# Kernel optimization log

Hardware: AMD Instinct MI355X
Metric: run time of the kernel (lower is better)

The kernel has to match this reference:

```python
import jax, jax.numpy as jnp
import numpy as np

C = 192; WS = 8; SHIFT = 4; NH = 6; HD = 32; N = WS * WS; EPS = 1e-5


def _cpb_table(ws):
    r = np.arange(-(ws - 1), ws, dtype=np.float32)
    t = np.stack(np.meshgrid(r, r, indexing='ij'), axis=-1) / (ws - 1) * 8.0
    t = np.sign(t) * np.log2(np.abs(t) + 1.0) / np.log2(8.0)
    return t.reshape(-1, 2)  # ((2ws-1)^2, 2)


def _rel_index(ws):
    c = np.stack(np.meshgrid(np.arange(ws), np.arange(ws), indexing='ij')).reshape(2, -1)
    rel = (c[:, :, None] - c[:, None, :]).transpose(1, 2, 0).astype(np.int64)
    rel[..., 0] += ws - 1; rel[..., 1] += ws - 1; rel[..., 0] *= 2 * ws - 1
    return rel.sum(-1)  # (N, N)


def _attn_mask(H, W, ws, shift):
    img = np.zeros((H, W), np.float32); cnt = 0.0
    sl = (slice(0, -ws), slice(-ws, -shift), slice(-shift, None))
    for hs in sl:
        for wsl in sl:
            img[hs, wsl] = cnt; cnt += 1.0
    m = img.reshape(H // ws, ws, W // ws, ws).transpose(0, 2, 1, 3).reshape(-1, ws * ws)
    d = m[:, None, :] - m[:, :, None]
    return np.where(d != 0, -100.0, 0.0).astype(np.float32)  # (nW, N, N)


def _ln(x, g, b):
    mu = jnp.mean(x, -1, keepdims=True)
    var = jnp.mean((x - mu) ** 2, -1, keepdims=True)
    return (x - mu) / jnp.sqrt(var + EPS) * g + b


def setup_inputs() -> dict:
    key = jax.random.key(0)
    ks = jax.random.split(key, 8)
    H = W = 384
    w = lambda k, s: jax.random.normal(k, s, jnp.float32) * 0.05
    return {
        'hidden_states': jax.random.normal(ks[0], (1, H * W, C), jnp.float32),
        'q_w': w(ks[1], (C, C)), 'q_b': jnp.zeros((C,), jnp.float32),
        'k_w': w(ks[2], (C, C)),
        'v_w': w(ks[3], (C, C)), 'v_b': jnp.zeros((C,), jnp.float32),
        'logit_scale': jnp.full((NH, 1, 1), np.log(10.0), jnp.float32),
        'cpb_w1': w(ks[4], (2, 512)), 'cpb_b1': jnp.zeros((512,), jnp.float32),
        'cpb_w2': w(ks[5], (512, NH)),
        'proj_w': w(ks[6], (C, C)), 'proj_b': jnp.zeros((C,), jnp.float32),
        'ln1_g': jnp.ones((C,), jnp.float32), 'ln1_b': jnp.zeros((C,), jnp.float32),
        'fc1_w': w(ks[7], (C, 2 * C)), 'fc1_b': jnp.zeros((2 * C,), jnp.float32),
        'fc2_w': w(jax.random.fold_in(key, 9), (2 * C, C)), 'fc2_b': jnp.zeros((C,), jnp.float32),
        'ln2_g': jnp.ones((C,), jnp.float32), 'ln2_b': jnp.zeros((C,), jnp.float32),
        'height': 384, 'width': 384,
    }


def reference(hidden_states, q_w, q_b, k_w, v_w, v_b, logit_scale, cpb_w1, cpb_b1,
              cpb_w2, proj_w, proj_b, ln1_g, ln1_b, fc1_w, fc1_b, fc2_w, fc2_b,
              ln2_g, ln2_b, height, width):
    B = hidden_states.shape[0]
    shortcut = hidden_states
    x = hidden_states.reshape(B, height, width, C)
    # shift
    x = jnp.roll(x, (-SHIFT, -SHIFT), (1, 2))
    # window partition -> (B*nW, N, C)
    win = x.reshape(B, height // WS, WS, width // WS, WS, C).transpose(0, 1, 3, 2, 4, 5).reshape(-1, N, C)
    q = (win @ q_w + q_b).reshape(-1, N, NH, HD).transpose(0, 2, 1, 3)
    k = (win @ k_w).reshape(-1, N, NH, HD).transpose(0, 2, 1, 3)
    v = (win @ v_w + v_b).reshape(-1, N, NH, HD).transpose(0, 2, 1, 3)
    # cosine attention
    qn = q / jnp.maximum(jnp.linalg.norm(q, axis=-1, keepdims=True), 1e-12)
    kn = k / jnp.maximum(jnp.linalg.norm(k, axis=-1, keepdims=True), 1e-12)
    scale = jnp.exp(jnp.minimum(logit_scale, jnp.log(100.0))).reshape(1, NH, 1, 1)
    scores = jnp.einsum('whnd,whmd->whnm', qn, kn) * scale
    # continuous relative position bias via MLP
    table = jnp.asarray(_cpb_table(WS))
    bias_tab = jax.nn.relu(table @ cpb_w1 + cpb_b1) @ cpb_w2  # (169, NH)
    idx = jnp.asarray(_rel_index(WS)).reshape(-1)
    rpb = bias_tab[idx].reshape(N, N, NH).transpose(2, 0, 1)
    rpb = 16.0 * jax.nn.sigmoid(rpb)
    mask = jnp.asarray(_attn_mask(height, width, WS, SHIFT))  # (nW, N, N)
    # NOTE: source adds the mask twice (faithful reproduction)
    scores = scores + rpb[None] + 2.0 * mask[:, None]
    probs = jax.nn.softmax(scores, -1)
    ctx = jnp.einsum('whnm,whmd->whnd', probs, v).transpose(0, 2, 1, 3).reshape(-1, N, C)
    attn = ctx @ proj_w + proj_b
    # window reverse + unshift
    x = attn.reshape(B, height // WS, width // WS, WS, WS, C).transpose(0, 1, 3, 2, 4, 5).reshape(B, height, width, C)
    x = jnp.roll(x, (SHIFT, SHIFT), (1, 2)).reshape(B, height * width, C)
    # post-norm residual (Swin v2 style)
    h = shortcut + _ln(x, ln1_g, ln1_b)
    mlp = jax.nn.gelu(h @ fc1_w + fc1_b, approximate=False) @ fc2_w + fc2_b
    return h + _ln(mlp, ln2_g, ln2_b)
```

## Files before the change

kernel.cpp:

```cpp
#include <hip/hip_runtime.h>
#include <hip/hip_bf16.h>
#include <math.h>

typedef __hip_bfloat16 bf16;
typedef __attribute__((ext_vector_type(8))) short short8;
typedef __attribute__((ext_vector_type(4))) float floatx4;
typedef unsigned int u32;

#define NTOK 147456
#define IMG 384

__device__ __forceinline__ int gather_row(int m) {
    int gw = m >> 6, t = m & 63;
    int wr = gw / 48, wc = gw - wr * 48;
    int hh = wr * 8 + (t >> 3);
    int ww = wc * 8 + (t & 7);
    int oh = hh + 4; if (oh >= IMG) oh -= IMG;
    int ow = ww + 4; if (ow >= IMG) ow -= IMG;
    return oh * IMG + ow;
}

__device__ __forceinline__ unsigned short f2bu(float f) {
    unsigned u = __float_as_uint(f);
    unsigned r = (u + 0x7fffu + ((u >> 16) & 1u)) >> 16;
    return (unsigned short)r;
}
__device__ __forceinline__ float bu2f(unsigned short u) {
    return __uint_as_float(((unsigned)u) << 16);
}

__device__ __forceinline__ float gelu_fast(float x) {
    const float z = fabsf(x) * 0.70710678118654752f;
    const float t = __builtin_amdgcn_rcpf(fmaf(0.3275911f, z, 1.0f));
    float p = fmaf(1.061405429f, t, -1.453152027f);
    p = fmaf(p, t, 1.421413741f);
    p = fmaf(p, t, -0.284496736f);
    p = fmaf(p, t, 0.254829592f);
    p *= t;
    const float e = __expf(-z * z);
    float erfv = fmaf(-p, e, 1.0f);
    erfv = (x < 0.0f) ? -erfv : erfv;
    return 0.5f * x * (1.0f + erfv);
}

__device__ __forceinline__ void async_copy16(void* lds, const void* g) {
    __builtin_amdgcn_global_load_lds(
        (const __attribute__((address_space(1))) u32*)g,
        (__attribute__((address_space(3))) u32*)lds,
        16, 0, 0);
}


__global__ __launch_bounds__(256)
void conv_pack(const float* __restrict__ hidden, bf16* __restrict__ Apk)
{
    const int cid = blockIdx.x * 256 + threadIdx.x;
    const int mtG = cid / 384;
    const int rest = cid - mtG * 384;
    const int kg = rest >> 4, mm = rest & 15;
    const int tok = mtG * 16 + mm;
    const float* p = hidden + (size_t)gather_row(tok) * 192 + kg * 8;
    const float4 a = *(const float4*)p;
    const float4 b = *(const float4*)(p + 4);
    short8 o;
    o[0] = (short)f2bu(a.x); o[1] = (short)f2bu(a.y);
    o[2] = (short)f2bu(a.z); o[3] = (short)f2bu(a.w);
    o[4] = (short)f2bu(b.x); o[5] = (short)f2bu(b.y);
    o[6] = (short)f2bu(b.z); o[7] = (short)f2bu(b.w);
    *(short8*)(Apk + (size_t)cid * 8) = o;
}

__global__ __launch_bounds__(256)
void pack_w(const float* __restrict__ W, bf16* __restrict__ out, int K, int N)
{
    const int cid = blockIdx.x * 256 + threadIdx.x;
    const int KG = K >> 3;
    const int total = (N >> 4) * KG * 16;
    if (cid >= total) return;
    const int n = cid & 15;
    const int kg = (cid >> 4) % KG;
    const int ntG = (cid >> 4) / KG;
    short8 o;
#pragma unroll
    for (int j = 0; j < 8; ++j)
        o[j] = (short)f2bu(W[(size_t)(kg * 8 + j) * N + ntG * 16 + n]);
    *(short8*)(out + (size_t)cid * 8) = o;
}

__global__ __launch_bounds__(256)
void fuse_bias(const float* __restrict__ qb, const float* __restrict__ vb,
               float* __restrict__ out)
{
    const int t = blockIdx.x * 256 + threadIdx.x;
    if (t >= 576) return;
    out[t] = (t < 192) ? qb[t] : ((t < 384) ? 0.0f : vb[t - 384]);
}

#define EPI_NONE 0
#define EPI_GELU 1

template<int KDIM, bool PACK_OUT, int EPI, int KGOUT, int MW>
__global__ __launch_bounds__(256, MW)
void gemm_mfma(const bf16* __restrict__ Apk, const bf16* __restrict__ Bpk,
               const float* __restrict__ bias, bf16* __restrict__ C, int N)
{
    constexpr int KG = KDIM / 8;
    constexpr int KT = KDIM / 32;
    constexpr int KC = KDIM / 192;
    __shared__ __align__(16) char sB[2][24576];
    const int tid = threadIdx.x;
    const int wave = tid >> 6, lane = tid & 63;
    const int bm = blockIdx.x * 128;
    const int NPo = N / 64;
    const char* Bsrc = (const char*)Bpk;

    short8 areg[2][KT];
    {
        const char* Asrc = (const char*)Apk;
#pragma unroll
        for (int x = 0; x < 2; ++x) {
            const size_t rowb = (size_t)((bm >> 4) + wave * 2 + x) * KG * 256;
#pragma unroll
            for (int kt = 0; kt < KT; ++kt)
                areg[x][kt] = *(const short8*)(Asrc + rowb + (size_t)kt * 1024 + lane * 16);
        }
    }

    auto stage = [&](int npo_, int kc_, int bufp) {
#pragma unroll
        for (int i = 0; i < 6; ++i) {
            const int cid = i * 256 + wave * 64 + lane;
            const int nt = cid / 384, off = cid - nt * 384;
            const char* g = Bsrc + ((size_t)((npo_ * 4 + nt) * KG + kc_ * 24) * 256 + (size_t)off * 16);
            async_copy16(sB[bufp] + (i * 256 + wave * 64) * 16, g);
        }
    };

    stage(0, 0, 0);

    for (int npo = 0; npo < NPo; ++npo) {
        floatx4 acc[8];
#pragma unroll
        for (int f = 0; f < 8; ++f)
            acc[f] = (floatx4){0.f, 0.f, 0.f, 0.f};

#pragma unroll
        for (int kc = 0; kc < KC; ++kc) {
            const int p = npo * KC + kc;
            const int buf = p & 1;
            const bool last = (npo == NPo - 1) && (kc == KC - 1);
            if (!last) {
                if (kc < KC - 1) stage(npo, kc + 1, buf ^ 1);
                else             stage(npo + 1, 0, buf ^ 1);
                asm volatile("s_waitcnt vmcnt(6)" ::: "memory");
            } else {
                asm volatile("s_waitcnt vmcnt(0)" ::: "memory");
            }
            __builtin_amdgcn_sched_barrier(0);
            asm volatile("s_barrier" ::: "memory");

            char* sb = sB[buf];
#pragma unroll
            for (int kt6 = 0; kt6 < 6; ++kt6) {
                const short8 a0 = areg[0][kc * 6 + kt6];
                const short8 a1 = areg[1][kc * 6 + kt6];
#pragma unroll
                for (int nt = 0; nt < 4; ++nt) {
                    const short8 b = *(const short8*)(sb + nt * 6144 + kt6 * 1024 + lane * 16);
                    acc[nt]     = __builtin_amdgcn_mfma_f32_16x16x32_bf16(a0, b, acc[nt],     0, 0, 0);
                    acc[4 + nt] = __builtin_amdgcn_mfma_f32_16x16x32_bf16(a1, b, acc[4 + nt], 0, 0, 0);
                }
            }
            if (kc < KC - 1)
                asm volatile("s_barrier" ::: "memory");
        }

        {
            const int ebuf = (npo * KC + KC - 1) & 1;
            asm volatile("s_barrier" ::: "memory");
            char* wb = sB[ebuf] + wave * 4608;
#pragma unroll
            for (int m2 = 0; m2 < 2; ++m2) {
#pragma unroll
                for (int nt = 0; nt < 4; ++nt) {
                    const floatx4 v = acc[m2 * 4 + nt];
                    const int c = nt * 16 + (lane & 15);
                    const float bval = bias ? bias[npo * 64 + c] : 0.0f;
#pragma unroll
                    for (int i = 0; i < 4; ++i) {
                        float f = v[i] + bval;
                        if (EPI == EPI_GELU)
                            f = gelu_fast(f);
                        const int r = m2 * 16 + (lane >> 4) * 4 + i;
                        *(unsigned short*)(wb + (r * 72 + c) * 2) = f2bu(f);
                    }
                }
            }
            asm volatile("s_waitcnt lgkmcnt(0)" ::: "memory");
            asm volatile("s_barrier" ::: "memory");
            if (PACK_OUT) {
                const int m = lane >> 1, c2 = (lane & 1) * 32;
                const int grow = bm + wave * 32 + m;
#pragma unroll
                for (int i = 0; i < 4; ++i) {
                    const short8 row = *(const short8*)(wb + (m * 72 + c2 + i * 8) * 2);
                    const int gcol = npo * 64 + c2 + i * 8;
                    bf16* dst = C + ((size_t)((grow >> 4) * KGOUT + (gcol >> 3)) * 16 + (grow & 15)) * 8;
                    *(short8*)dst = row;
                }
            } else {
                const int mr = lane >> 3, c2 = (lane & 7) * 8;
#pragma unroll
                for (int i = 0; i < 4; ++i) {
                    const int rr = i * 8 + mr;
                    const short8 row = *(const short8*)(wb + (rr * 72 + c2) * 2);
                    bf16* dst = C + (size_t)(bm + wave * 32 + rr) * N + npo * 64 + c2;
                    *(short8*)dst = row;
                }
            }
            asm volatile("s_barrier" ::: "memory");
        }
    }
}


__device__ __forceinline__ float cpb_coord(int i) {
    float a = (float)(i - 7) * (8.0f / 7.0f);
    float s = (a > 0.f) ? 1.f : ((a < 0.f) ? -1.f : 0.f);
    return s * log2f(fabsf(a) + 1.0f) * (1.0f / 3.0f);
}

__global__ __launch_bounds__(512)
void cpb_mlp(const float* __restrict__ w1, const float* __restrict__ b1,
             const float* __restrict__ w2, float* __restrict__ tab)
{
    const int r = blockIdx.x;
    const int t = threadIdx.x;
    const float x0 = cpb_coord(r / 15);
    const float x1 = cpb_coord(r % 15);
    const float hgt = fmaxf(x0 * w1[t] + x1 * w1[512 + t] + b1[t], 0.0f);
    __shared__ float red[512];
    for (int n = 0; n < 6; ++n) {
        red[t] = hgt * w2[t * 6 + n];
        __syncthreads();
        for (int s = 256; s > 0; s >>= 1) {
            if (t < s) red[t] += red[t + s];
            __syncthreads();
        }
        if (t == 0) tab[r * 6 + n] = red[0];
        __syncthreads();
    }
}

__global__ __launch_bounds__(256)
void rpb_expand(const float* __restrict__ tab, float* __restrict__ rpb)
{
    const int idx = blockIdx.x * 256 + threadIdx.x;
    if (idx >= 6 * 4096) return;
    const int h = idx >> 12;
    const int t = (idx >> 6) & 63;
    const int j = idx & 63;
    const int pr = t >> 3, pc = t & 7, qr = j >> 3, qc = j & 7;
    const int ridx = (pr - qr + 7) * 15 + (pc - qc + 7);
    const float v = tab[ridx * 6 + h];
    rpb[idx] = 16.0f / (1.0f + expf(-v));
}

__global__ __launch_bounds__(256, 2)
void attn_mfma(const bf16* __restrict__ QKV, const float* __restrict__ rpb,
               const float* __restrict__ logit_scale, bf16* __restrict__ Ctx)
{
    __shared__ __align__(16) char lds[4][9216];
    const int wave = threadIdx.x >> 6, lane = threadIdx.x & 63;
    const int l15 = lane & 15, quad = lane >> 4;
    const int wh = blockIdx.x * 4 + wave;
    const int w = wh / 6, h = wh - w * 6;
    char* Pb = lds[wave];
    char* Vt = lds[wave] + 4608;

    const bf16* wbase = QKV + (size_t)w * 64 * 576;

    {
        const bf16* vp = wbase + (size_t)lane * 576 + 384 + h * 32;
        const short8 v0 = *(const short8*)(vp);
        const short8 v1 = *(const short8*)(vp + 8);
        const short8 v2 = *(const short8*)(vp + 16);
        const short8 v3 = *(const short8*)(vp + 24);
#pragma unroll
        for (int j = 0; j < 8; ++j) {
            *(short*)(Vt + ((j     ) * 72 + lane) * 2) = v0[j];
            *(short*)(Vt + ((j +  8) * 72 + lane) * 2) = v1[j];
            *(short*)(Vt + ((j + 16) * 72 + lane) * 2) = v2[j];
            *(short*)(Vt + ((j + 24) * 72 + lane) * 2) = v3[j];
        }
    }

    const int wr = w / 48, wc = w - wr * 48;
    const bool edge = (wr == 47) || (wc == 47);
    int rid_j[4];
    if (edge) {
#pragma unroll
        for (int jt = 0; jt < 4; ++jt) {
            const int t = jt * 16 + l15;
            const int rr = (wr == 47) ? (((t >> 3) < 4) ? 1 : 2) : 0;
            const int rc = (wc == 47) ? (((t & 7) < 4) ? 1 : 2) : 0;
            rid_j[jt] = rr * 3 + rc;
        }
    }

    short8 bfrag[4];
#pragma unroll
    for (int jt = 0; jt < 4; ++jt) {
        const short8 raw = *(const short8*)(wbase + (size_t)(jt * 16 + l15) * 576 + 192 + h * 32 + quad * 8);
        float f[8]; float ss = 0.f;
#pragma unroll
        for (int j = 0; j < 8; ++j) { f[j] = bu2f((unsigned short)raw[j]); ss += f[j] * f[j]; }
        ss += __shfl_xor(ss, 16); ss += __shfl_xor(ss, 32);
        const float rn = 1.0f / fmaxf(sqrtf(ss), 1e-12f);
        short8 o;
#pragma unroll
        for (int j = 0; j < 8; ++j) o[j] = (short)f2bu(f[j] * rn);
        bfrag[jt] = o;
    }

    floatx4 acc[4][4];
#pragma unroll
    for (int it = 0; it < 4; ++it)
#pragma unroll
        for (int jt = 0; jt < 4; ++jt)
            acc[it][jt] = (floatx4){0.f, 0.f, 0.f, 0.f};
#pragma unroll
    for (int it = 0; it < 4; ++it) {
        const short8 raw = *(const short8*)(wbase + (size_t)(it * 16 + l15) * 576 + h * 32 + quad * 8);
        float f[8]; float ss = 0.f;
#pragma unroll
        for (int j = 0; j < 8; ++j) { f[j] = bu2f((unsigned short)raw[j]); ss += f[j] * f[j]; }
        ss += __shfl_xor(ss, 16); ss += __shfl_xor(ss, 32);
        const float rn = 1.0f / fmaxf(sqrtf(ss), 1e-12f);
        short8 afr;
#pragma unroll
        for (int j = 0; j < 8; ++j) afr[j] = (short)f2bu(f[j] * rn);
#pragma unroll
        for (int jt = 0; jt < 4; ++jt)
            acc[it][jt] = __builtin_amdgcn_mfma_f32_16x16x32_bf16(afr, bfrag[jt], acc[it][jt], 0, 0, 0);
    }

    const float scale = __expf(fminf(logit_scale[h], 4.6051701859880914f));
    const float* rpbh = rpb + h * 4096;

#pragma unroll
    for (int it = 0; it < 4; ++it) {
#pragma unroll
        for (int r = 0; r < 4; ++r) {
            const int i = it * 16 + quad * 4 + r;
            int rid_i = 0;
            if (edge) {
                const int rr = (wr == 47) ? (((i >> 3) < 4) ? 1 : 2) : 0;
                const int rc = (wc == 47) ? (((i & 7) < 4) ? 1 : 2) : 0;
                rid_i = rr * 3 + rc;
            }
#pragma unroll
            for (int jt = 0; jt < 4; ++jt) {
                float v = acc[it][jt][r] * scale + rpbh[i * 64 + jt * 16 + l15];
                if (edge && rid_i != rid_j[jt]) v -= 200.0f;
                acc[it][jt][r] = v;
            }
        }
    }

    float inv[4][4];
#pragma unroll
    for (int it = 0; it < 4; ++it) {
#pragma unroll
        for (int r = 0; r < 4; ++r) {
            float m = fmaxf(fmaxf(acc[it][0][r], acc[it][1][r]),
                            fmaxf(acc[it][2][r], acc[it][3][r]));
            m = fmaxf(m, __shfl_xor(m, 1)); m = fmaxf(m, __shfl_xor(m, 2));
            m = fmaxf(m, __shfl_xor(m, 4)); m = fmaxf(m, __shfl_xor(m, 8));
            float s = 0.f;
#pragma unroll
            for (int jt = 0; jt < 4; ++jt) {
                const float e = __expf(acc[it][jt][r] - m);
                acc[it][jt][r] = e; s += e;
            }
            s += __shfl_xor(s, 1); s += __shfl_xor(s, 2);
            s += __shfl_xor(s, 4); s += __shfl_xor(s, 8);
            inv[it][r] = 1.0f / s;
        }
    }

    floatx4 ctx[4][2];
#pragma unroll
    for (int it = 0; it < 4; ++it)
#pragma unroll
        for (int dt = 0; dt < 2; ++dt)
            ctx[it][dt] = (floatx4){0.f, 0.f, 0.f, 0.f};

#pragma unroll
    for (int ks = 0; ks < 2; ++ks) {
#pragma unroll
        for (int it = 0; it < 4; ++it)
#pragma unroll
            for (int jl = 0; jl < 2; ++jl)
#pragma unroll
                for (int r = 0; r < 4; ++r) {
                    const int i = it * 16 + quad * 4 + r;
                    *(short*)(Pb + (i * 36 + jl * 16 + l15) * 2) =
                        (short)f2bu(acc[it][ks * 2 + jl][r]);
                }
#pragma unroll
        for (int it = 0; it < 4; ++it) {
            const short8 pf = *(const short8*)(Pb + ((it * 16 + l15) * 36 + quad * 8) * 2);
#pragma unroll
            for (int dt = 0; dt < 2; ++dt) {
                const short8 vf = *(const short8*)(Vt + ((dt * 16 + l15) * 72 + ks * 32 + quad * 8) * 2);
                ctx[it][dt] = __builtin_amdgcn_mfma_f32_16x16x32_bf16(pf, vf, ctx[it][dt], 0, 0, 0);
            }
        }
    }

#pragma unroll
    for (int it = 0; it < 4; ++it)
#pragma unroll
        for (int dt = 0; dt < 2; ++dt)
#pragma unroll
            for (int r = 0; r < 4; ++r) {
                const int i = it * 16 + quad * 4 + r;
                *(short*)(Pb + (i * 36 + dt * 16 + l15) * 2) =
                    (short)f2bu(ctx[it][dt][r] * inv[it][r]);
            }

    const int tok = w * 64 + lane;
    const size_t obase = ((size_t)(tok >> 4) * 24 + h * 4) * 128 + (size_t)(tok & 15) * 8;
#pragma unroll
    for (int c = 0; c < 4; ++c) {
        const short8 row = *(const short8*)(Pb + (lane * 36 + c * 8) * 2);
        *(short8*)(Ctx + obase + (size_t)c * 128) = row;
    }
}


__global__ __launch_bounds__(256)
void ln_h(const bf16* __restrict__ X, const float* __restrict__ hidden,
          const float* __restrict__ g, const float* __restrict__ b,
          bf16* __restrict__ Hres, bf16* __restrict__ Hpk)
{
    const int lane = threadIdx.x & 63;
    const int wv = threadIdx.x >> 6;
    const int tok = blockIdx.x * 4 + wv;
    const int grow = gather_row(tok);
    __shared__ float rows[4][192];
    const bf16* xr = X + (size_t)tok * 192;
    const float x0 = bu2f(*(const unsigned short*)(xr + lane));
    const float x1 = bu2f(*(const unsigned short*)(xr + lane + 64));
    const float x2 = bu2f(*(const unsigned short*)(xr + lane + 128));
    float s = x0 + x1 + x2;
#pragma unroll
    for (int o = 32; o > 0; o >>= 1) s += __shfl_xor(s, o);
    const float mean = s * (1.0f / 192.0f);
    const float d0 = x0 - mean, d1 = x1 - mean, d2 = x2 - mean;
    float vsum = d0 * d0 + d1 * d1 + d2 * d2;
#pragma unroll
    for (int o = 32; o > 0; o >>= 1) vsum += __shfl_xor(vsum, o);
    const float rstd = rsqrtf(vsum * (1.0f / 192.0f) + 1e-5f);
    const float* hr = hidden + (size_t)grow * 192;
    const float h0 = hr[lane]       + d0 * rstd * g[lane]       + b[lane];
    const float h1 = hr[lane + 64]  + d1 * rstd * g[lane + 64]  + b[lane + 64];
    const float h2 = hr[lane + 128] + d2 * rstd * g[lane + 128] + b[lane + 128];
    bf16* hres = Hres + (size_t)tok * 192;
    *(unsigned short*)(hres + lane)       = f2bu(h0);
    *(unsigned short*)(hres + lane + 64)  = f2bu(h1);
    *(unsigned short*)(hres + lane + 128) = f2bu(h2);
    rows[wv][lane] = h0; rows[wv][lane + 64] = h1; rows[wv][lane + 128] = h2;
    __syncthreads();
    if (lane < 24) {
        short8 o;
#pragma unroll
        for (int j = 0; j < 8; ++j) o[j] = (short)f2bu(rows[wv][lane * 8 + j]);
        const int mtG = tok >> 4, mm = tok & 15;
        *(short8*)(Hpk + ((size_t)(mtG * 24 + lane) * 16 + mm) * 8) = o;
    }
}

__global__ __launch_bounds__(256)
void ln_out(const bf16* __restrict__ Y, const bf16* __restrict__ Hres,
            const float* __restrict__ g, const float* __restrict__ b,
            float* __restrict__ Out)
{
    const int lane = threadIdx.x & 63;
    const int tok = blockIdx.x * 4 + (threadIdx.x >> 6);
    const int grow = gather_row(tok);
    const bf16* yr = Y + (size_t)tok * 192;
    const float x0 = bu2f(*(const unsigned short*)(yr + lane));
    const float x1 = bu2f(*(const unsigned short*)(yr + lane + 64));
    const float x2 = bu2f(*(const unsigned short*)(yr + lane + 128));
    float s = x0 + x1 + x2;
#pragma unroll
    for (int o = 32; o > 0; o >>= 1) s += __shfl_xor(s, o);
    const float mean = s * (1.0f / 192.0f);
    const float d0 = x0 - mean, d1 = x1 - mean, d2 = x2 - mean;
    float vsum = d0 * d0 + d1 * d1 + d2 * d2;
#pragma unroll
    for (int o = 32; o > 0; o >>= 1) vsum += __shfl_xor(vsum, o);
    const float rstd = rsqrtf(vsum * (1.0f / 192.0f) + 1e-5f);
    const bf16* hr = Hres + (size_t)tok * 192;
    float* op = Out + (size_t)grow * 192;
    op[lane]       = bu2f(*(const unsigned short*)(hr + lane))       + d0 * rstd * g[lane]       + b[lane];
    op[lane + 64]  = bu2f(*(const unsigned short*)(hr + lane + 64))  + d1 * rstd * g[lane + 64]  + b[lane + 64];
    op[lane + 128] = bu2f(*(const unsigned short*)(hr + lane + 128)) + d2 * rstd * g[lane + 128] + b[lane + 128];
}


extern "C" void kernel_launch(void* const* d_in, const int* in_sizes, int n_in,
                              void* d_out, int out_size, void* d_ws, size_t ws_size,
                              hipStream_t stream)
{
    const float* hidden = (const float*)d_in[0];
    const float* q_w = (const float*)d_in[1];
    const float* q_b = (const float*)d_in[2];
    const float* k_w = (const float*)d_in[3];
    const float* v_w = (const float*)d_in[4];
    const float* v_b = (const float*)d_in[5];
    const float* logit_scale = (const float*)d_in[6];
    const float* cpb_w1 = (const float*)d_in[7];
    const float* cpb_b1 = (const float*)d_in[8];
    const float* cpb_w2 = (const float*)d_in[9];
    const float* proj_w = (const float*)d_in[10];
    const float* proj_b = (const float*)d_in[11];
    const float* ln1_g = (const float*)d_in[12];
    const float* ln1_b = (const float*)d_in[13];
    const float* fc1_w = (const float*)d_in[14];
    const float* fc1_b = (const float*)d_in[15];
    const float* fc2_w = (const float*)d_in[16];
    const float* fc2_b = (const float*)d_in[17];
    const float* ln2_g = (const float*)d_in[18];
    const float* ln2_b = (const float*)d_in[19];

    char* ws = (char*)d_ws;
    bf16*  APK   = (bf16*)(ws + 0);
    float* RPB   = (float*)(ws + 0);
    bf16*  PROJW = (bf16*)(ws + (1 << 20));
    bf16*  MID   = (bf16*)(ws + 0);
    bf16*  CTX   = (bf16*)(ws + 56623104);
    bf16*  QKVW  = (bf16*)(ws + 56623104);
    float* QKVB  = (float*)(ws + 56844288);
    float* TAB   = (float*)(ws + 56846592);
    bf16*  QKV   = (bf16*)(ws + 113246208);
    bf16*  HRES  = (bf16*)(ws + 113246208);
    bf16*  HPK   = (bf16*)(ws + 169869312);
    bf16*  Y     = (bf16*)(ws + 226492416);
    bf16*  X     = (bf16*)(ws + 283115520);
    bf16*  FC1W  = (bf16*)(ws + 283115520);
    bf16*  FC2W  = (bf16*)(ws + 283262976);
    float* OUT   = (float*)d_out;

    cpb_mlp<<<225, 512, 0, stream>>>(cpb_w1, cpb_b1, cpb_w2, TAB);
    fuse_bias<<<3, 256, 0, stream>>>(q_b, v_b, QKVB);
    pack_w<<<18, 256, 0, stream>>>(q_w, QKVW,                 192, 192);
    pack_w<<<18, 256, 0, stream>>>(k_w, QKVW + 12 * 24 * 128, 192, 192);
    pack_w<<<18, 256, 0, stream>>>(v_w, QKVW + 24 * 24 * 128, 192, 192);
    conv_pack<<<13824, 256, 0, stream>>>(hidden, APK);

    gemm_mfma<192, false, EPI_NONE, 1, 3><<<1152, 256, 0, stream>>>(APK, QKVW, QKVB, QKV, 576);

    rpb_expand<<<96, 256, 0, stream>>>(TAB, RPB);
    pack_w<<<18, 256, 0, stream>>>(proj_w, PROJW, 192, 192);

    attn_mfma<<<3456, 256, 0, stream>>>(QKV, RPB, logit_scale, CTX);

    gemm_mfma<192, false, EPI_NONE, 1, 3><<<1152, 256, 0, stream>>>(CTX, PROJW, proj_b, X, 192);

    ln_h<<<NTOK / 4, 256, 0, stream>>>(X, hidden, ln1_g, ln1_b, HRES, HPK);

    pack_w<<<36, 256, 0, stream>>>(fc1_w, FC1W, 192, 384);
    pack_w<<<36, 256, 0, stream>>>(fc2_w, FC2W, 384, 192);

    gemm_mfma<192, true, EPI_GELU, 48, 3><<<1152, 256, 0, stream>>>(HPK, FC1W, fc1_b, MID, 384);
    gemm_mfma<384, false, EPI_NONE, 1, 2><<<1152, 256, 0, stream>>>(MID, FC2W, fc2_b, Y, 192);

    ln_out<<<NTOK / 4, 256, 0, stream>>>(Y, HRES, ln2_g, ln2_b, OUT);
}
```

Before: 652.7 us.

## Fold q/k normalization into scores and drop softmax max pass

The attention kernel no longer normalizes Q and K in registers before the MFMA. It feeds raw bf16 Q/K and applies the row and column inverse norms and the logit scale to the score afterwards. The softmax max-reduction is replaced by a constant shift (scale+16) precomputed into the rpb table, which is valid because cosine scores are bounded. Packed bf16 conversions replace scalar rounding, and the GEMM waitcnt thresholds are relaxed to overlap more loads. This trades some accuracy (unnormalized bf16 inputs, fixed softmax offset) for fewer ALU ops and shuffles.

```diff
diff --git a/kernel.cpp b/kernel.cpp
--- a/kernel.cpp
+++ b/kernel.cpp
@@ -27,6 +27,12 @@
 }
 __device__ __forceinline__ float bu2f(unsigned short u) {
     return __uint_as_float(((unsigned)u) << 16);
+}
+
+__device__ __forceinline__ u32 cvt_pk_bf16(float lo, float hi) {
+    u32 r;
+    asm("v_cvt_pk_bf16_f32 %0, %1, %2" : "=v"(r) : "v"(lo), "v"(hi));
+    return r;
 }
 
 __device__ __forceinline__ float gelu_fast(float x) {
@@ -152,9 +158,13 @@
             if (!last) {
                 if (kc < KC - 1) stage(npo, kc + 1, buf ^ 1);
                 else             stage(npo + 1, 0, buf ^ 1);
-                asm volatile("s_waitcnt vmcnt(6)" ::: "memory");
+                if (kc == 0 && npo > 0)
+                    asm volatile("s_waitcnt vmcnt(10)" ::: "memory");
+                else
+                    asm volatile("s_waitcnt vmcnt(6)" ::: "memory");
             } else {
-                asm volatile("s_waitcnt vmcnt(0)" ::: "memory");
+                if (KC == 1) asm volatile("s_waitcnt vmcnt(4)" ::: "memory");
+                else         asm volatile("s_waitcnt vmcnt(0)" ::: "memory");
             }
             __builtin_amdgcn_sched_barrier(0);
             asm volatile("s_barrier" ::: "memory");
@@ -253,7 +263,8 @@
 }
 
 __global__ __launch_bounds__(256)
-void rpb_expand(const float* __restrict__ tab, float* __restrict__ rpb)
+void rpb_expand(const float* __restrict__ tab, const float* __restrict__ logit_scale,
+                float* __restrict__ rpb)
 {
     const int idx = blockIdx.x * 256 + threadIdx.x;
     if (idx >= 6 * 4096) return;
@@ -263,7 +274,8 @@
     const int pr = t >> 3, pc = t & 7, qr = j >> 3, qc = j & 7;
     const int ridx = (pr - qr + 7) * 15 + (pc - qc + 7);
     const float v = tab[ridx * 6 + h];
-    rpb[idx] = 16.0f / (1.0f + expf(-v));
+    const float scale = __expf(fminf(logit_scale[h], 4.6051701859880914f));
+    rpb[idx] = 16.0f / (1.0f + expf(-v)) - scale - 16.0f;
 }
 
 __global__ __launch_bounds__(256, 2)
@@ -308,22 +320,25 @@
         }
     }
 
-    short8 bfrag[4];
+    const float scale = __expf(fminf(logit_scale[h], 4.6051701859880914f));
+
+    short8 kfr[4];
+    float rnk[4];
 #pragma unroll
     for (int jt = 0; jt < 4; ++jt) {
-        const short8 raw = *(const short8*)(wbase + (size_t)(jt * 16 + l15) * 576 + 192 + h * 32 + quad * 8);
-        float f[8]; float ss = 0.f;
-#pragma unroll
-        for (int j = 0; j < 8; ++j) { f[j] = bu2f((unsigned short)raw[j]); ss += f[j] * f[j]; }
+        kfr[jt] = *(const short8*)(wbase + (size_t)(jt * 16 + l15) * 576 + 192 + h * 32 + quad * 8);
+        float ss = 0.f;
+#pragma unroll
+        for (int j = 0; j < 8; ++j) {
+            const float f = bu2f((unsigned short)kfr[jt][j]);
+            ss = fmaf(f, f, ss);
+        }
         ss += __shfl_xor(ss, 16); ss += __shfl_xor(ss, 32);
-        const float rn = 1.0f / fmaxf(sqrtf(ss), 1e-12f);
-        short8 o;
-#pragma unroll
-        for (int j = 0; j < 8; ++j) o[j] = (short)f2bu(f[j] * rn);
-        bfrag[jt] = o;
+        rnk[jt] = __builtin_amdgcn_rcpf(fmaxf(__builtin_amdgcn_sqrtf(ss), 1e-12f));
     }
 
     floatx4 acc[4][4];
+    float rnq[4];
 #pragma unroll
     for (int it = 0; it < 4; ++it)
 #pragma unroll
@@ -331,61 +346,46 @@
             acc[it][jt] = (floatx4){0.f, 0.f, 0.f, 0.f};
 #pragma unroll
     for (int it = 0; it < 4; ++it) {
-        const short8 raw = *(const short8*)(wbase + (size_t)(it * 16 + l15) * 576 + h * 32 + quad * 8);
-        float f[8]; float ss = 0.f;
-#pragma unroll
-        for (int j = 0; j < 8; ++j) { f[j] = bu2f((unsigned short)raw[j]); ss += f[j] * f[j]; }
+        const short8 qf = *(const short8*)(wbase + (size_t)(it * 16 + l15) * 576 + h * 32 + quad * 8);
+        float ss = 0.f;
+#pragma unroll
+        for (int j = 0; j < 8; ++j) {
+            const float f = bu2f((unsigned short)qf[j]);
+            ss = fmaf(f, f, ss);
+        }
         ss += __shfl_xor(ss, 16); ss += __shfl_xor(ss, 32);
-        const float rn = 1.0f / fmaxf(sqrtf(ss), 1e-12f);
-        short8 afr;
-#pragma unroll
-        for (int j = 0; j < 8; ++j) afr[j] = (short)f2bu(f[j] * rn);
+        rnq[it] = scale * __builtin_amdgcn_rcpf(fmaxf(__builtin_amdgcn_sqrtf(ss), 1e-12f));
 #pragma unroll
         for (int jt = 0; jt < 4; ++jt)
-            acc[it][jt] = __builtin_amdgcn_mfma_f32_16x16x32_bf16(afr, bfrag[jt], acc[it][jt], 0, 0, 0);
-    }
-
-    const float scale = __expf(fminf(logit_scale[h], 4.6051701859880914f));
+            acc[it][jt] = __builtin_amdgcn_mfma_f32_16x16x32_bf16(qf, kfr[jt], acc[it][jt], 0, 0, 0);
+    }
+
     const float* rpbh = rpb + h * 4096;
 
+    float inv[4][4];
 #pragma unroll
     for (int it = 0; it < 4; ++it) {
 #pragma unroll
         for (int r = 0; r < 4; ++r) {
             const int i = it * 16 + quad * 4 + r;
+            const float rq = __shfl(rnq[it], quad * 4 + r);
             int rid_i = 0;
             if (edge) {
                 const int rr = (wr == 47) ? (((i >> 3) < 4) ? 1 : 2) : 0;
                 const int rc = (wc == 47) ? (((i & 7) < 4) ? 1 : 2) : 0;
                 rid_i = rr * 3 + rc;
             }
+            float s = 0.f;
 #pragma unroll
             for (int jt = 0; jt < 4; ++jt) {
-                float v = acc[it][jt][r] * scale + rpbh[i * 64 + jt * 16 + l15];
+                float v = fmaf(acc[it][jt][r], rq * rnk[jt], rpbh[i * 64 + jt * 16 + l15]);
                 if (edge && rid_i != rid_j[jt]) v -= 200.0f;
-                acc[it][jt][r] = v;
-            }
-        }
-    }
-
-    float inv[4][4];
-#pragma unroll
-    for (int it = 0; it < 4; ++it) {
-#pragma unroll
-        for (int r = 0; r < 4; ++r) {
-            float m = fmaxf(fmaxf(acc[it][0][r], acc[it][1][r]),
-                            fmaxf(acc[it][2][r], acc[it][3][r]));
-            m = fmaxf(m, __shfl_xor(m, 1)); m = fmaxf(m, __shfl_xor(m, 2));
-            m = fmaxf(m, __shfl_xor(m, 4)); m = fmaxf(m, __shfl_xor(m, 8));
-            float s = 0.f;
-#pragma unroll
-            for (int jt = 0; jt < 4; ++jt) {
-                const float e = __expf(acc[it][jt][r] - m);
+                const float e = __expf(v);
                 acc[it][jt][r] = e; s += e;
             }
             s += __shfl_xor(s, 1); s += __shfl_xor(s, 2);
             s += __shfl_xor(s, 4); s += __shfl_xor(s, 8);
-            inv[it][r] = 1.0f / s;
+            inv[it][r] = __builtin_amdgcn_rcpf(s);
         }
     }
 
@@ -401,13 +401,12 @@
 #pragma unroll
         for (int it = 0; it < 4; ++it)
 #pragma unroll
-            for (int jl = 0; jl < 2; ++jl)
-#pragma unroll
-                for (int r = 0; r < 4; ++r) {
-                    const int i = it * 16 + quad * 4 + r;
-                    *(short*)(Pb + (i * 36 + jl * 16 + l15) * 2) =
-                        (short)f2bu(acc[it][ks * 2 + jl][r]);
-                }
+            for (int r = 0; r < 4; ++r) {
+                const int i = it * 16 + quad * 4 + r;
+                const u32 pk = cvt_pk_bf16(acc[it][ks * 2][r], acc[it][ks * 2 + 1][r]);
+                *(short*)(Pb + (i * 36 + l15) * 2)      = (short)pk;
+                *(short*)(Pb + (i * 36 + 16 + l15) * 2) = (short)(pk >> 16);
+            }
 #pragma unroll
         for (int it = 0; it < 4; ++it) {
             const short8 pf = *(const short8*)(Pb + ((it * 16 + l15) * 36 + quad * 8) * 2);
@@ -422,13 +421,12 @@
 #pragma unroll
     for (int it = 0; it < 4; ++it)
 #pragma unroll
-        for (int dt = 0; dt < 2; ++dt)
-#pragma unroll
-            for (int r = 0; r < 4; ++r) {
-                const int i = it * 16 + quad * 4 + r;
-                *(short*)(Pb + (i * 36 + dt * 16 + l15) * 2) =
-                    (short)f2bu(ctx[it][dt][r] * inv[it][r]);
-            }
+        for (int r = 0; r < 4; ++r) {
+            const int i = it * 16 + quad * 4 + r;
+            const u32 pk = cvt_pk_bf16(ctx[it][0][r] * inv[it][r], ctx[it][1][r] * inv[it][r]);
+            *(short*)(Pb + (i * 36 + l15) * 2)      = (short)pk;
+            *(short*)(Pb + (i * 36 + 16 + l15) * 2) = (short)(pk >> 16);
+        }
 
     const int tok = w * 64 + lane;
     const size_t obase = ((size_t)(tok >> 4) * 24 + h * 4) * 128 + (size_t)(tok & 15) * 8;
@@ -563,7 +561,7 @@
 
     gemm_mfma<192, false, EPI_NONE, 1, 3><<<1152, 256, 0, stream>>>(APK, QKVW, QKVB, QKV, 576);
 
-    rpb_expand<<<96, 256, 0, stream>>>(TAB, RPB);
+    rpb_expand<<<96, 256, 0, stream>>>(TAB, logit_scale, RPB);
     pack_w<<<18, 256, 0, stream>>>(proj_w, PROJW, 192, 192);
 
     attn_mfma<<<3456, 256, 0, stream>>>(QKV, RPB, logit_scale, CTX);
```

Result: slower. 670.0 us (+2.7%).
